# Kernel tuning notes

Hardware: AMD Instinct MI355X
Metric: run time of the kernel (lower is better)

The kernel has to match this reference:

```python
import jax, jax.numpy as jnp
import numpy as np

B, L, D, N = 4, 1024, 1024, 16
HD = D // N
DFF = 4 * D
EPS = 1e-5


def _ln(x, g, b):
    m = jnp.mean(x, axis=-1, keepdims=True)
    v = jnp.mean(jnp.square(x - m), axis=-1, keepdims=True)
    return (x - m) * jax.lax.rsqrt(v + EPS) * g + b


def setup_inputs() -> dict:
    key = jax.random.key(0)
    ks = jax.random.split(key, 8)
    s = 0.02
    return {
        "x": jax.random.normal(ks[0], (B, L, D), jnp.float32),
        "decay": jax.random.uniform(ks[1], (N, L, L), jnp.float32),
        "ln1_g": jnp.ones((D,), jnp.float32),
        "ln1_b": jnp.zeros((D,), jnp.float32),
        "proj_W": jax.random.normal(ks[2], (4 * D, D), jnp.float32) * s,
        "proj_b": jnp.zeros((4 * D,), jnp.float32),
        "reto_W": jax.random.normal(ks[3], (D, D), jnp.float32) * s,
        "reto_b": jnp.zeros((D,), jnp.float32),
        "ln2_g": jnp.ones((D,), jnp.float32),
        "ln2_b": jnp.zeros((D,), jnp.float32),
        "ffn1_W": jax.random.normal(ks[4], (DFF, D), jnp.float32) * s,
        "ffn1_b": jnp.zeros((DFF,), jnp.float32),
        "ffn2_W": jax.random.normal(ks[5], (D, DFF), jnp.float32) * s,
        "ffn2_b": jnp.zeros((D,), jnp.float32),
    }


def reference(x, decay, ln1_g, ln1_b, proj_W, proj_b, reto_W, reto_b,
              ln2_g, ln2_b, ffn1_W, ffn1_b, ffn2_W, ffn2_b):
    ln_x = _ln(x, ln1_g, ln1_b)
    p = ln_x @ proj_W.T + proj_b                      # [B, L, 4D]
    q, k, v, xo = jnp.split(p, 4, axis=-1)            # each [B, L, D]

    def heads(t):  # [B, L, D] -> [B, N, L, HD]
        return t.reshape(B, L, N, HD).transpose(0, 2, 1, 3)

    q, k, v = heads(q), heads(k), heads(v)
    scores = jnp.einsum('bnld,bnmd->bnlm', q, k) * decay[None]  # [B,N,L,L]
    ret = jnp.einsum('bnlm,bnmd->bnld', scores, v)              # [B,N,L,HD]
    ret = ret.transpose(0, 2, 1, 3).reshape(B, L, D)
    ret = ret * jax.nn.silu(xo)                                  # gated
    ret = ret @ reto_W.T + reto_b
    x = x + ret
    h = _ln(x, ln2_g, ln2_b)
    h = jax.nn.gelu(h @ ffn1_W.T + ffn1_b, approximate=False) @ ffn2_W.T + ffn2_b
    return x + h
```

## Files before the change

### kernel.cpp

```cpp
#include <hip/hip_runtime.h>


typedef _Float16 f16;
typedef _Float16 f16x8 __attribute__((ext_vector_type(8)));
typedef float floatx4 __attribute__((ext_vector_type(4)));

#define EP_BIAS_F16      0
#define EP_DECAY_F16     1
#define EP_BIAS_GELU_F16 2
#define EP_PARTIAL_F32   3

template <bool F32> struct out_sel { typedef f16 T; };
template <> struct out_sel<true>   { typedef float T; };

__device__ __forceinline__ void gload_lds16(const void* g, void* s) {
    __builtin_amdgcn_global_load_lds(
        (const __attribute__((address_space(1))) unsigned int*)g,
        (__attribute__((address_space(3))) unsigned int*)s, 16, 0, 0);
}

__device__ __forceinline__ float erf_fast(float x) {
    const float ax = fabsf(x);
    const float t  = __builtin_amdgcn_rcpf(1.f + 0.3275911f * ax);
    const float p  = t * (0.254829592f + t * (-0.284496736f + t * (1.421413741f +
                     t * (-1.453152027f + t * 1.061405429f))));
    const float r  = 1.f - p * __expf(-ax * ax);
    return copysignf(r, x);
}

__global__ __launch_bounds__(256, 2) void attn_fused(
    const f16* __restrict__ p, const f16* __restrict__ vT,
    const float* __restrict__ decay, f16* __restrict__ gated)
{
    const int y  = blockIdx.y;
    const int bp = y >> 4, h = y & 15;
    const int m0 = blockIdx.x * 64;

    __shared__ __align__(16) f16 Kb[4][64 * 64];
    __shared__ __align__(16) f16 Vb[4][64 * 64];
    __shared__ __align__(16) f16 Ss[4][16 * 68];

    const int t    = threadIdx.x;
    const int lane = t & 63;
    const int w    = t >> 6;
    const int quad = lane >> 4;
    const int fr   = lane & 15;
    const int wq0  = w * 16;

    const int b0 = bp * 2, b1 = b0 + 1;
    const f16*   Qg0 = p + (size_t)(b0 * 1024 + m0) * 4096 + h * 64;
    const f16*   Qg1 = p + (size_t)(b1 * 1024 + m0) * 4096 + h * 64;
    const f16*   Kg0 = p + (size_t)(b0 * 1024) * 4096 + 1024 + h * 64;
    const f16*   Kg1 = p + (size_t)(b1 * 1024) * 4096 + 1024 + h * 64;
    const f16*   Vg0 = vT + (size_t)(b0 * 16 + h) * 65536;
    const f16*   Vg1 = vT + (size_t)(b1 * 16 + h) * 65536;
    const f16*   XOg0 = p + (size_t)(b0 * 1024 + m0) * 4096 + 3072 + h * 64;
    const f16*   XOg1 = p + (size_t)(b1 * 1024 + m0) * 4096 + 3072 + h * 64;
    const float* Dg  = decay + (size_t)h * 1048576 + (size_t)m0 * 1024;

    f16x8 q00, q01, q10, q11;
    {
        const size_t qrow = (size_t)(wq0 + fr) * 4096;
        q00 = *(const f16x8*)(Qg0 + qrow + (0 * 4 + quad) * 8);
        q01 = *(const f16x8*)(Qg0 + qrow + (1 * 4 + quad) * 8);
        q10 = *(const f16x8*)(Qg1 + qrow + (0 * 4 + quad) * 8);
        q11 = *(const f16x8*)(Qg1 + qrow + (1 * 4 + quad) * 8);
    }

    floatx4 oa0[4] = {}, oa1[4] = {};
    float dA[16], dB[16];

    const float* Dt = Dg + (size_t)(wq0 + quad * 4) * 1024 + fr;

#define DLOAD(dst, jj) { _Pragma("unroll") \
    for (int tn = 0; tn < 4; ++tn) { _Pragma("unroll") \
      for (int r = 0; r < 4; ++r) \
        dst[tn * 4 + r] = Dt[(size_t)r * 1024 + (jj) + tn * 16]; } \
    __builtin_amdgcn_sched_barrier(0); }

#define STAGE(Kgp, Vgp, jj, pb) { _Pragma("unroll") \
    for (int i_ = 0; i_ < 2; ++i_) { \
      const int ci = t + i_ * 256; \
      const int r_ = ci >> 3; \
      const int c_ = ((ci & 7) ^ (r_ & 7)) * 8; \
      gload_lds16((Kgp) + (size_t)((jj) + r_) * 4096 + c_, &Kb[pb][ci * 8]); \
      gload_lds16((Vgp) + (size_t)r_ * 1024 + (jj) + c_, &Vb[pb][ci * 8]); \
    } }

#define VMBAR(N) { asm volatile("s_waitcnt vmcnt(" #N ")" ::: "memory"); \
    __builtin_amdgcn_s_barrier(); __builtin_amdgcn_sched_barrier(0); }

#define STEP(qa, qb, oa, dreg, pb) { \
    floatx4 sa[4] = {}; \
    _Pragma("unroll") \
    for (int kc = 0; kc < 2; ++kc) { \
      const int cc = kc * 4 + quad; \
      f16x8 bf[4]; \
      _Pragma("unroll") \
      for (int tn = 0; tn < 4; ++tn) { \
        const int kv = tn * 16 + fr; \
        bf[tn] = *(const f16x8*)&Kb[pb][(kv * 8 + (cc ^ (kv & 7))) * 8]; \
      } \
      _Pragma("unroll") \
      for (int tn = 0; tn < 4; ++tn) \
        sa[tn] = __builtin_amdgcn_mfma_f32_16x16x32_f16(kc ? (qb) : (qa), bf[tn], sa[tn], 0, 0, 0); \
    } \
    _Pragma("unroll") \
    for (int tn = 0; tn < 4; ++tn) { _Pragma("unroll") \
      for (int r = 0; r < 4; ++r) \
        Ss[w][(quad * 4 + r) * 68 + tn * 16 + fr] = (f16)(sa[tn][r] * dreg[tn * 4 + r]); } \
    _Pragma("unroll") \
    for (int kc = 0; kc < 2; ++kc) { \
      const int cc = kc * 4 + quad; \
      const f16x8 af = *(const f16x8*)&Ss[w][fr * 68 + cc * 8]; \
      f16x8 bf[4]; \
      _Pragma("unroll") \
      for (int tn = 0; tn < 4; ++tn) { \
        const int d = tn * 16 + fr; \
        bf[tn] = *(const f16x8*)&Vb[pb][(d * 8 + (cc ^ (d & 7))) * 8]; \
      } \
      _Pragma("unroll") \
      for (int tn = 0; tn < 4; ++tn) \
        oa[tn] = __builtin_amdgcn_mfma_f32_16x16x32_f16(af, bf[tn], oa[tn], 0, 0, 0); \
    } }

#define EPILOG(oa, XOgp, bq) { \
    _Pragma("unroll") \
    for (int tn = 0; tn < 4; ++tn) { _Pragma("unroll") \
      for (int r = 0; r < 4; ++r) { \
        const int qrow = wq0 + quad * 4 + r; \
        const int d = tn * 16 + fr; \
        float g = (float)XOgp[(size_t)qrow * 4096 + d]; \
        g = g * __builtin_amdgcn_rcpf(1.f + __expf(-g)); \
        Ss[w][(quad * 4 + r) * 68 + tn * 16 + fr] = (f16)(oa[tn][r] * g); \
      } } \
    f16* Og = gated + (size_t)((bq) * 1024 + m0 + wq0) * 1024 + h * 64; \
    _Pragma("unroll") \
    for (int i = 0; i < 2; ++i) { \
      const int jj = lane + i * 64; \
      const int rr = jj >> 3; \
      const int cc = jj & 7; \
      const uint2 lo = *(const uint2*)&Ss[w][rr * 68 + cc * 8]; \
      const uint2 hi = *(const uint2*)&Ss[w][rr * 68 + cc * 8 + 4]; \
      uint4 val = make_uint4(lo.x, lo.y, hi.x, hi.y); \
      *(uint4*)(Og + (size_t)rr * 1024 + cc * 8) = val; \
    } }

    DLOAD(dA, 0);
    STAGE(Kg0, Vg0, 0, 0);
    STAGE(Kg1, Vg1, 0, 1);
    VMBAR(4);

    for (int i = 0; i < 7; ++i) {
        const int j1 = i * 128 + 64;
        const int j2 = i * 128 + 128;
        DLOAD(dB, j1);
        STAGE(Kg0, Vg0, j1, 2);
        STEP(q00, q01, oa0, dA, 0);
        VMBAR(4);
        STAGE(Kg1, Vg1, j1, 3);
        STEP(q10, q11, oa1, dA, 1);
        VMBAR(4);
        DLOAD(dA, j2);
        STAGE(Kg0, Vg0, j2, 0);
        STEP(q00, q01, oa0, dB, 2);
        VMBAR(4);
        STAGE(Kg1, Vg1, j2, 1);
        STEP(q10, q11, oa1, dB, 3);
        VMBAR(4);
    }
    {
        DLOAD(dB, 960);
        STAGE(Kg0, Vg0, 960, 2);
        STEP(q00, q01, oa0, dA, 0);
        VMBAR(4);
        STAGE(Kg1, Vg1, 960, 3);
        STEP(q10, q11, oa1, dA, 1);
        VMBAR(4);
        STEP(q00, q01, oa0, dB, 2);
        VMBAR(0);
        STEP(q10, q11, oa1, dB, 3);
    }

    EPILOG(oa0, XOg0, b0);
    EPILOG(oa1, XOg1, b1);

#undef DLOAD
#undef STAGE
#undef VMBAR
#undef STEP
#undef EPILOG
}

template <int BM, int BN, int WM, int WN, int EP, int XSWZ>
__global__ __launch_bounds__(256, 4) void gemm_bt(
    const f16* __restrict__ A, const f16* __restrict__ B, void* __restrict__ Cv,
    int M, int N, int K, int lda, int ldb, int ldc,
    long long sAo, long long sAi, long long sBo, long long sBi,
    long long sCo, long long sCi, int inner,
    int nsplit, int Kc, long long sCk,
    const float* __restrict__ bias,
    const void* __restrict__ aux, long long sXo, long long sXi, int ldaux)
{
    constexpr bool OUT_F32 = (EP == EP_PARTIAL_F32);
    typedef typename out_sel<OUT_F32>::T OutT;
    constexpr int ESIZE       = OUT_F32 ? 4 : 2;
    constexpr int CSTRIDE     = BN + 4;
    constexpr int TILE_BYTES  = (BM + BN) * 64 * 2;
    constexpr int STAGE_BYTES = OUT_F32 ? 0 : BM * CSTRIDE * ESIZE;
    constexpr int SMEM_BYTES  = TILE_BYTES > STAGE_BYTES ? TILE_BYTES : STAGE_BYTES;

    __shared__ __align__(16) char smem[SMEM_BYTES];
    f16*  As = (f16*)smem;
    f16*  Bs = (f16*)(smem + BM * 128);
    OutT* Cs = (OutT*)smem;

    int z = blockIdx.z;
    const int ks = z % nsplit; z /= nsplit;
    const int zo = z / inner, zi = z % inner;
    A += zo * sAo + zi * sAi;
    B += zo * sBo + zi * sBi;
    const long long cOff = (long long)zo * sCo + (long long)zi * sCi + (long long)ks * sCk;
    const long long xOff = (long long)zo * sXo + (long long)zi * sXi;

    int bx = blockIdx.x, by = blockIdx.y;
    if constexpr (XSWZ) {
        const int gx  = gridDim.x;
        const int nb  = gx * gridDim.y;
        const int lin = bx + gx * by;
        const int nlin = (lin & 7) * (nb >> 3) + (lin >> 3);
        bx = nlin % gx;
        by = nlin / gx;
    }
    const int m0 = by * BM;
    const int n0 = bx * BN;

    const int t    = threadIdx.x;
    const int lane = t & 63;
    const int w    = t >> 6;
    const int wm   = (w >> 1) * (WM * 16);
    const int wn   = (w & 1) * (WN * 16);
    const int fr   = lane & 15;
    const int quad = lane >> 4;

    constexpr int ACH = BM / 32;
    constexpr int BCH = BN / 32;

    floatx4 acc[WM][WN] = {};

    const int kbeg = ks * Kc, kend = kbeg + Kc;
    for (int kk = kbeg; kk < kend; kk += 64) {
#pragma unroll
        for (int i = 0; i < ACH; ++i) {
            const int ci = t + i * 256;
            const int r  = ci >> 3;
            const int c  = ((ci & 7) ^ (r & 7)) * 8;
            gload_lds16(A + (size_t)(m0 + r) * lda + kk + c, &As[ci * 8]);
        }
#pragma unroll
        for (int i = 0; i < BCH; ++i) {
            const int ci = t + i * 256;
            const int r  = ci >> 3;
            const int c  = ((ci & 7) ^ (r & 7)) * 8;
            gload_lds16(B + (size_t)(n0 + r) * ldb + kk + c, &Bs[ci * 8]);
        }
        __syncthreads();

#pragma unroll
        for (int kh = 0; kh < 2; ++kh) {
            const int cc = kh * 4 + quad;
            f16x8 af[WM], bf[WN];
#pragma unroll
            for (int tm = 0; tm < WM; ++tm) {
                const int r = wm + tm * 16 + fr;
                af[tm] = *(const f16x8*)&As[(r * 8 + (cc ^ (r & 7))) * 8];
            }
#pragma unroll
            for (int tn = 0; tn < WN; ++tn) {
                const int r = wn + tn * 16 + fr;
                bf[tn] = *(const f16x8*)&Bs[(r * 8 + (cc ^ (r & 7))) * 8];
            }
#pragma unroll
            for (int tm = 0; tm < WM; ++tm)
#pragma unroll
                for (int tn = 0; tn < WN; ++tn)
                    acc[tm][tn] = __builtin_amdgcn_mfma_f32_16x16x32_f16(af[tm], bf[tn], acc[tm][tn], 0, 0, 0);
        }
        __syncthreads();
    }

    const int er = quad * 4;
    const int ec = lane & 15;
    if constexpr (OUT_F32) {
        float* Pg = (float*)Cv + cOff;
#pragma unroll
        for (int tm = 0; tm < WM; ++tm)
#pragma unroll
            for (int tn = 0; tn < WN; ++tn)
#pragma unroll
                for (int r = 0; r < 4; ++r) {
                    const int grow = m0 + wm + tm * 16 + er + r;
                    const int gcol = n0 + wn + tn * 16 + ec;
                    Pg[(size_t)grow * ldc + gcol] = acc[tm][tn][r];
                }
        return;
    }

#pragma unroll
    for (int tm = 0; tm < WM; ++tm) {
#pragma unroll
        for (int tn = 0; tn < WN; ++tn) {
#pragma unroll
            for (int r = 0; r < 4; ++r) {
                const int lrow = wm + tm * 16 + er + r;
                const int col  = wn + tn * 16 + ec;
                const int grow = m0 + lrow;
                const int gcol = n0 + col;
                const float v = acc[tm][tn][r];
                float val;
                if constexpr (EP == EP_BIAS_F16) {
                    val = v + bias[gcol];
                } else if constexpr (EP == EP_DECAY_F16) {
                    const float* dk = (const float*)aux + xOff;
                    val = v * dk[(size_t)grow * ldaux + gcol];
                } else if constexpr (EP == EP_BIAS_GELU_F16) {
                    const float u = v + bias[gcol];
                    val = 0.5f * u * (1.f + erf_fast(u * 0.70710678118f));
                } else {
                    val = v;
                }
                Cs[lrow * CSTRIDE + col] = (OutT)val;
            }
        }
    }
    __syncthreads();

    constexpr int PER_ROW = BN * ESIZE / 16;
    constexpr int NCHUNK  = (BM * PER_ROW) / 256;
#pragma unroll
    for (int i = 0; i < NCHUNK; ++i) {
        const int j  = t + i * 256;
        const int rr = j / PER_ROW;
        const int cc = j - rr * PER_ROW;
        const char* src = smem + (size_t)rr * (CSTRIDE * ESIZE) + (size_t)cc * 16;
        const uint2 lo = *(const uint2*)src;
        const uint2 hi = *(const uint2*)(src + 8);
        uint4 val = make_uint4(lo.x, lo.y, hi.x, hi.y);
        char* dst = (char*)Cv +
            (size_t)(cOff + (long long)(m0 + rr) * ldc + n0) * ESIZE +
            (size_t)cc * 16;
        *(uint4*)dst = val;
    }
}

__global__ __launch_bounds__(256) void reduce2_bias_res(
    const float4* __restrict__ P, const float* __restrict__ bias,
    const float4* __restrict__ res, float4* __restrict__ out)
{
    const int i = blockIdx.x * 256 + threadIdx.x;
    const int col4 = i & 255;
    const float4 a = P[i];
    const float4 b = P[i + 1048576];
    const float4 r = res[i];
    const float4 bi = ((const float4*)bias)[col4];
    float4 o;
    o.x = a.x + b.x + r.x + bi.x;
    o.y = a.y + b.y + r.y + bi.y;
    o.z = a.z + b.z + r.z + bi.z;
    o.w = a.w + b.w + r.w + bi.w;
    out[i] = o;
}

__global__ __launch_bounds__(256) void ln_to_f16(
    const float* __restrict__ x, const float* __restrict__ g,
    const float* __restrict__ b, f16* __restrict__ out)
{
    const int row = blockIdx.x;
    const int t = threadIdx.x;
    const float4 xv = ((const float4*)(x + (size_t)row * 1024))[t];
    float s  = xv.x + xv.y + xv.z + xv.w;
    float ss = xv.x * xv.x + xv.y * xv.y + xv.z * xv.z + xv.w * xv.w;
    for (int o = 32; o > 0; o >>= 1) {
        s  += __shfl_down(s, o, 64);
        ss += __shfl_down(ss, o, 64);
    }
    __shared__ float red[8];
    const int wv = t >> 6;
    if ((t & 63) == 0) { red[wv] = s; red[wv + 4] = ss; }
    __syncthreads();
    s  = red[0] + red[1] + red[2] + red[3];
    ss = red[4] + red[5] + red[6] + red[7];
    const float mean = s * (1.f / 1024.f);
    const float var  = ss * (1.f / 1024.f) - mean * mean;
    const float rstd = rsqrtf(var + 1e-5f);
    const float4 gv = ((const float4*)g)[t];
    const float4 bv = ((const float4*)b)[t];
    alignas(8) f16 h[4];
    h[0] = (f16)((xv.x - mean) * rstd * gv.x + bv.x);
    h[1] = (f16)((xv.y - mean) * rstd * gv.y + bv.y);
    h[2] = (f16)((xv.z - mean) * rstd * gv.z + bv.z);
    h[3] = (f16)((xv.w - mean) * rstd * gv.w + bv.w);
    ((uint2*)(out + (size_t)row * 1024))[t] = *(uint2*)h;
}

__global__ __launch_bounds__(256) void cast_f32_f16(
    const float* __restrict__ in, f16* __restrict__ out, int n4)
{
    const int i = blockIdx.x * 256 + threadIdx.x;
    if (i < n4) {
        const float4 v = ((const float4*)in)[i];
        alignas(8) f16 h[4] = {(f16)v.x, (f16)v.y, (f16)v.z, (f16)v.w};
        ((uint2*)out)[i] = *(uint2*)h;
    }
}

__global__ __launch_bounds__(256) void transpose_v(
    const f16* __restrict__ p, f16* __restrict__ vT)
{
    const int z = blockIdx.y;
    const int b = z >> 4, h = z & 15;
    const int m0 = blockIdx.x * 64;
    __shared__ f16 tile[64][72];
    const int t = threadIdx.x;
    const f16* src = p + (size_t)(b * 1024 + m0) * 4096 + 2048 + h * 64;
#pragma unroll
    for (int pass = 0; pass < 4; ++pass) {
        const int r = (t >> 4) + pass * 16;
        const int c = (t & 15) * 4;
        *(uint2*)&tile[r][c] = *(const uint2*)(src + (size_t)r * 4096 + c);
    }
    __syncthreads();
    f16* dst = vT + (size_t)z * 65536 + m0;
#pragma unroll
    for (int pass = 0; pass < 4; ++pass) {
        const int d  = (t >> 4) + pass * 16;
        const int mc = (t & 15) * 4;
        alignas(8) f16 tmp[4] = {tile[mc][d], tile[mc + 1][d], tile[mc + 2][d], tile[mc + 3][d]};
        *(uint2*)(dst + (size_t)d * 1024 + mc) = *(uint2*)tmp;
    }
}

extern "C" void kernel_launch(void* const* d_in, const int* in_sizes, int n_in,
                              void* d_out, int out_size, void* d_ws, size_t ws_size,
                              hipStream_t stream) {
    const float* x      = (const float*)d_in[0];
    const float* decay  = (const float*)d_in[1];
    const float* ln1_g  = (const float*)d_in[2];
    const float* ln1_b  = (const float*)d_in[3];
    const float* proj_W = (const float*)d_in[4];
    const float* proj_b = (const float*)d_in[5];
    const float* reto_W = (const float*)d_in[6];
    const float* reto_b = (const float*)d_in[7];
    const float* ln2_g  = (const float*)d_in[8];
    const float* ln2_b  = (const float*)d_in[9];
    const float* ffn1_W = (const float*)d_in[10];
    const float* ffn1_b = (const float*)d_in[11];
    const float* ffn2_W = (const float*)d_in[12];
    const float* ffn2_b = (const float*)d_in[13];
    float* out = (float*)d_out;

    char* w = (char*)d_ws;
    auto alloc = [&](size_t bytes) { char* r = w; w += (bytes + 255) & ~(size_t)255; return r; };
    f16*   Wp   = (f16*)alloc((size_t)4096 * 1024 * 2);
    f16*   Wr   = (f16*)alloc((size_t)1024 * 1024 * 2);
    f16*   W1   = (f16*)alloc((size_t)4096 * 1024 * 2);
    f16*   W2   = (f16*)alloc((size_t)1024 * 4096 * 2);
    f16*   buf8 = (f16*)alloc((size_t)4096 * 1024 * 2);
    f16*   p    = (f16*)alloc((size_t)4096 * 4096 * 2);
    f16*   S    = (f16*)alloc((size_t)16 * 1024 * 1024 * 2);
    float* y    = (float*)alloc((size_t)4096 * 1024 * 4);

    f16*   lnx   = buf8;
    f16*   vT    = buf8;
    f16*   hln   = buf8;
    f16*   gated = Wp;
    f16*   ffh   = p;
    float* Pk    = (float*)S;

    cast_f32_f16<<<4096, 256, 0, stream>>>(proj_W, Wp, 1048576);
    cast_f32_f16<<<1024, 256, 0, stream>>>(reto_W, Wr, 262144);
    cast_f32_f16<<<4096, 256, 0, stream>>>(ffn1_W, W1, 1048576);
    cast_f32_f16<<<4096, 256, 0, stream>>>(ffn2_W, W2, 1048576);

    ln_to_f16<<<4096, 256, 0, stream>>>(x, ln1_g, ln1_b, lnx);

    gemm_bt<128, 128, 4, 4, EP_BIAS_F16, 0><<<dim3(32, 32, 1), 256, 0, stream>>>(
        lnx, Wp, p, 4096, 4096, 1024, 1024, 1024, 4096,
        0, 0, 0, 0, 0, 0, 1, 1, 1024, 0, proj_b, nullptr, 0, 0, 0);

    transpose_v<<<dim3(16, 64), 256, 0, stream>>>(p, vT);

    attn_fused<<<dim3(16, 32), 256, 0, stream>>>(p, vT, decay, gated);

    gemm_bt<128, 128, 4, 4, EP_PARTIAL_F32, 1><<<dim3(8, 32, 2), 256, 0, stream>>>(
        gated, Wr, Pk, 4096, 1024, 1024, 1024, 1024, 1024,
        0, 0, 0, 0, 0, 0, 1, 2, 512, 4194304, nullptr, nullptr, 0, 0, 0);
    reduce2_bias_res<<<4096, 256, 0, stream>>>(
        (const float4*)Pk, reto_b, (const float4*)x, (float4*)y);

    ln_to_f16<<<4096, 256, 0, stream>>>(y, ln2_g, ln2_b, hln);

    gemm_bt<128, 128, 4, 4, EP_BIAS_GELU_F16, 0><<<dim3(32, 32, 1), 256, 0, stream>>>(
        hln, W1, ffh, 4096, 4096, 1024, 1024, 1024, 4096,
        0, 0, 0, 0, 0, 0, 1, 1, 1024, 0, ffn1_b, nullptr, 0, 0, 0);

    gemm_bt<128, 128, 4, 4, EP_PARTIAL_F32, 1><<<dim3(8, 32, 2), 256, 0, stream>>>(
        ffh, W2, Pk, 4096, 1024, 4096, 4096, 4096, 1024,
        0, 0, 0, 0, 0, 0, 1, 2, 2048, 4194304, nullptr, nullptr, 0, 0, 0);
    reduce2_bias_res<<<4096, 256, 0, stream>>>(
        (const float4*)Pk, ffn2_b, (const float4*)y, (float4*)out);
}
```

Before: 395.8 us.

## Store projection output in head-tiled layout and retile V transpose

```diff
diff --git a/kernel.cpp b/kernel.cpp
--- a/kernel.cpp
+++ b/kernel.cpp
@@ -48,19 +48,20 @@
     const int wq0  = w * 16;
 
     const int b0 = bp * 2, b1 = b0 + 1;
-    const f16*   Qg0 = p + (size_t)(b0 * 1024 + m0) * 4096 + h * 64;
-    const f16*   Qg1 = p + (size_t)(b1 * 1024 + m0) * 4096 + h * 64;
-    const f16*   Kg0 = p + (size_t)(b0 * 1024) * 4096 + 1024 + h * 64;
-    const f16*   Kg1 = p + (size_t)(b1 * 1024) * 4096 + 1024 + h * 64;
-    const f16*   Vg0 = vT + (size_t)(b0 * 16 + h) * 65536;
-    const f16*   Vg1 = vT + (size_t)(b1 * 16 + h) * 65536;
-    const f16*   XOg0 = p + (size_t)(b0 * 1024 + m0) * 4096 + 3072 + h * 64;
-    const f16*   XOg1 = p + (size_t)(b1 * 1024 + m0) * 4096 + 3072 + h * 64;
+    const int z0 = b0 * 16 + h, z1 = z0 + 16;
+    const f16*   Qg0 = p + ((size_t)h * 4096 + b0 * 1024 + m0) * 64;
+    const f16*   Qg1 = p + ((size_t)h * 4096 + b1 * 1024 + m0) * 64;
+    const f16*   Kg0 = p + ((size_t)(16 + h) * 4096 + b0 * 1024) * 64;
+    const f16*   Kg1 = p + ((size_t)(16 + h) * 4096 + b1 * 1024) * 64;
+    const f16*   Vg0 = vT + (size_t)z0 * 65536;
+    const f16*   Vg1 = vT + (size_t)z1 * 65536;
+    const f16*   XOg0 = p + ((size_t)(48 + h) * 4096 + b0 * 1024 + m0) * 64;
+    const f16*   XOg1 = p + ((size_t)(48 + h) * 4096 + b1 * 1024 + m0) * 64;
     const float* Dg  = decay + (size_t)h * 1048576 + (size_t)m0 * 1024;
 
     f16x8 q00, q01, q10, q11;
     {
-        const size_t qrow = (size_t)(wq0 + fr) * 4096;
+        const size_t qrow = (size_t)(wq0 + fr) * 64;
         q00 = *(const f16x8*)(Qg0 + qrow + (0 * 4 + quad) * 8);
         q01 = *(const f16x8*)(Qg0 + qrow + (1 * 4 + quad) * 8);
         q10 = *(const f16x8*)(Qg1 + qrow + (0 * 4 + quad) * 8);
@@ -83,8 +84,8 @@
       const int ci = t + i_ * 256; \
       const int r_ = ci >> 3; \
       const int c_ = ((ci & 7) ^ (r_ & 7)) * 8; \
-      gload_lds16((Kgp) + (size_t)((jj) + r_) * 4096 + c_, &Kb[pb][ci * 8]); \
-      gload_lds16((Vgp) + (size_t)r_ * 1024 + (jj) + c_, &Vb[pb][ci * 8]); \
+      gload_lds16((Kgp) + (size_t)(jj) * 64 + r_ * 64 + c_, &Kb[pb][ci * 8]); \
+      gload_lds16((Vgp) + (size_t)(jj) * 64 + r_ * 64 + c_, &Vb[pb][ci * 8]); \
     } }
 
 #define VMBAR(N) { asm volatile("s_waitcnt vmcnt(" #N ")" ::: "memory"); \
@@ -130,7 +131,7 @@
       for (int r = 0; r < 4; ++r) { \
         const int qrow = wq0 + quad * 4 + r; \
         const int d = tn * 16 + fr; \
-        float g = (float)XOgp[(size_t)qrow * 4096 + d]; \
+        float g = (float)XOgp[(size_t)qrow * 64 + d]; \
         g = g * __builtin_amdgcn_rcpf(1.f + __expf(-g)); \
         Ss[w][(quad * 4 + r) * 68 + tn * 16 + fr] = (f16)(oa[tn][r] * g); \
       } } \
@@ -192,7 +193,7 @@
 #undef EPILOG
 }
 
-template <int BM, int BN, int WM, int WN, int EP, int XSWZ>
+template <int BM, int BN, int WM, int WN, int EP, int XSWZ, int PTILED = 0>
 __global__ __launch_bounds__(256, 4) void gemm_bt(
     const f16* __restrict__ A, const f16* __restrict__ B, void* __restrict__ Cv,
     int M, int N, int K, int lda, int ldb, int ldc,
@@ -346,9 +347,16 @@
         const uint2 lo = *(const uint2*)src;
         const uint2 hi = *(const uint2*)(src + 8);
         uint4 val = make_uint4(lo.x, lo.y, hi.x, hi.y);
-        char* dst = (char*)Cv +
-            (size_t)(cOff + (long long)(m0 + rr) * ldc + n0) * ESIZE +
-            (size_t)cc * 16;
+        char* dst;
+        if constexpr (PTILED) {
+            const int gc0 = n0 + cc * 8;
+            dst = (char*)Cv +
+                (((size_t)(gc0 >> 6) * 4096 + (m0 + rr)) * 64 + (gc0 & 63)) * 2;
+        } else {
+            dst = (char*)Cv +
+                (size_t)(cOff + (long long)(m0 + rr) * ldc + n0) * ESIZE +
+                (size_t)cc * 16;
+        }
         *(uint4*)dst = val;
     }
 }
@@ -422,21 +430,21 @@
     const int m0 = blockIdx.x * 64;
     __shared__ f16 tile[64][72];
     const int t = threadIdx.x;
-    const f16* src = p + (size_t)(b * 1024 + m0) * 4096 + 2048 + h * 64;
+    const f16* src = p + ((size_t)(32 + h) * 4096 + b * 1024 + m0) * 64;
 #pragma unroll
     for (int pass = 0; pass < 4; ++pass) {
         const int r = (t >> 4) + pass * 16;
         const int c = (t & 15) * 4;
-        *(uint2*)&tile[r][c] = *(const uint2*)(src + (size_t)r * 4096 + c);
+        *(uint2*)&tile[r][c] = *(const uint2*)(src + (size_t)r * 64 + c);
     }
     __syncthreads();
-    f16* dst = vT + (size_t)z * 65536 + m0;
+    f16* dst = vT + (size_t)z * 65536 + (size_t)(m0 >> 6) * 4096;
 #pragma unroll
     for (int pass = 0; pass < 4; ++pass) {
         const int d  = (t >> 4) + pass * 16;
         const int mc = (t & 15) * 4;
         alignas(8) f16 tmp[4] = {tile[mc][d], tile[mc + 1][d], tile[mc + 2][d], tile[mc + 3][d]};
-        *(uint2*)(dst + (size_t)d * 1024 + mc) = *(uint2*)tmp;
+        *(uint2*)(dst + (size_t)d * 64 + mc) = *(uint2*)tmp;
     }
 }
 
@@ -484,7 +492,7 @@
 
     ln_to_f16<<<4096, 256, 0, stream>>>(x, ln1_g, ln1_b, lnx);
 
-    gemm_bt<128, 128, 4, 4, EP_BIAS_F16, 0><<<dim3(32, 32, 1), 256, 0, stream>>>(
+    gemm_bt<128, 128, 4, 4, EP_BIAS_F16, 1, 1><<<dim3(32, 32, 1), 256, 0, stream>>>(
         lnx, Wp, p, 4096, 4096, 1024, 1024, 1024, 4096,
         0, 0, 0, 0, 0, 0, 1, 1, 1024, 0, proj_b, nullptr, 0, 0, 0);
 
@@ -500,7 +508,7 @@
 
     ln_to_f16<<<4096, 256, 0, stream>>>(y, ln2_g, ln2_b, hln);
 
-    gemm_bt<128, 128, 4, 4, EP_BIAS_GELU_F16, 0><<<dim3(32, 32, 1), 256, 0, stream>>>(
+    gemm_bt<128, 128, 4, 4, EP_BIAS_GELU_F16, 1><<<dim3(32, 32, 1), 256, 0, stream>>>(
         hln, W1, ffh, 4096, 4096, 1024, 1024, 1024, 4096,
         0, 0, 0, 0, 0, 0, 1, 1, 1024, 0, ffn1_b, nullptr, 0, 0, 0);
 
```

Result: no change. 390.8 us (-1.3%).
